# Performance work log

Measured on AMD Instinct MI355X. Metric: run time of the kernel, lower is better.

Reference implementation:

```python
import jax, jax.numpy as jnp
import numpy as np

WINDOW_SIZES = (1, 2, 3)
ALPHA = 0.2          # LeakyReLU negative slope
NEG = -9e15          # mask fill value from the torch code


def _xavier(key, shape, gain=np.sqrt(2.0)):
    fan_in, fan_out = shape[0], shape[1]
    std = gain * np.sqrt(2.0 / (fan_in + fan_out))
    return jax.random.normal(key, shape, jnp.float32) * std


def setup_inputs() -> dict:
    key = jax.random.key(0)
    k1, k2, k3, k4, k5 = jax.random.split(key, 5)
    T, B, D, F = 512, 64, 256, 256  # turns, batch, input_dim, output_dim (must match)
    return {
        "local_semantic_vectors": jax.random.normal(k1, (T, B, D), jnp.float32),
        "input_turns": jax.random.randint(k2, (B,), 0, T),  # turns[bt] <= T-1
        "W": _xavier(k3, (D, F)),
        "a1": _xavier(k4, (F, 1)),
        "a2": _xavier(k5, (F, 1)),
    }


def _window_mean(x, w):
    # x: [B, T, D] -> sliding-window mean over axis 1 (window w), zero-padded at end.
    B, T, D = x.shape
    xp = jnp.pad(x, ((0, 0), (0, w - 1), (0, 0)))
    acc = xp[:, :T]
    for j in range(1, w):  # w <= 3, tiny unrolled loop
        acc = acc + xp[:, j:j + T]
    return acc / w


def reference(local_semantic_vectors, input_turns, W, a1, a2):
    # local_semantic_vectors: [T, B, D] -> [B, T, D]
    x = jnp.swapaxes(local_semantic_vectors, 0, 1)
    B, T, D = x.shape
    t_idx = jnp.arange(T)

    num = jnp.zeros((B, W.shape[1]), jnp.float32)
    vws = jnp.zeros((B,), jnp.float32)  # number of window sizes with cnt > 0

    for w in WINDOW_SIZES:
        # number of valid windows per sample: t runs while w+t-1 <= turns
        cnt = jnp.maximum(input_turns - w + 2, 0)                  # [B]
        valid = t_idx[None, :] < cnt[:, None]                      # [B, T]

        # pooled window vectors, zero beyond cnt (max_turn padded to T;
        # padded rows are fully masked and dropped, so the result matches)
        pooled = jnp.where(valid[:, :, None], _window_mean(x, w), 0.0)  # [B, T, D]

        # GAT-style masked self-attention
        h = pooled @ W                                             # [B, T, F]
        f1 = h @ a1                                                # [B, T, 1]
        f2 = h @ a2                                                # [B, T, 1]
        e = jax.nn.leaky_relu(f1 + jnp.swapaxes(f2, 1, 2), ALPHA)  # [B, T, T]
        mask = valid[:, :, None] & valid[:, None, :]
        attn = jax.nn.softmax(jnp.where(mask, e, NEG), axis=-1)
        h_prime = attn @ h                                         # [B, T, F]

        # mean over the first cnt rows
        denom = jnp.maximum(cnt, 1).astype(jnp.float32)
        inter = (h_prime * valid[:, :, None]).sum(axis=1) / denom[:, None]  # [B, F]

        has = (cnt > 0).astype(jnp.float32)
        num = num + inter * has[:, None]
        vws = vws + has

    # cnt is non-increasing in w, so windows with cnt>0 are exactly the first vws;
    # vws >= 1 always (w=1 gives cnt = turns + 2 >= 2).
    return num / vws[:, None]
```

## Files before the change

kernel.cpp:

```cpp
#include <hip/hip_runtime.h>
#include <math.h>

#define T_DIM 512
#define B_DIM 64
#define D_DIM 256
#define F_DIM 256
#define ALPHA 0.2f
#define L2E 1.44269504089f
#define NEGL -1.0e38f

#define U_OFF 0
#define V_OFF 256
#define P_OFF 512
#define Q_OFF (P_OFF + T_DIM * B_DIM)
#define GG_OFF (Q_OFF + T_DIM * B_DIM)

__global__ __launch_bounds__(256) void g_uv(const float* __restrict__ W,
                                            const float* __restrict__ a1,
                                            const float* __restrict__ a2,
                                            float* __restrict__ ws) {
    int tid = threadIdx.x;
    int wave = tid >> 6, lane = tid & 63;
    int d = blockIdx.x * 4 + wave;
    float4 wv = ((const float4*)(W + (size_t)d * F_DIM))[lane];
    float4 a1v = ((const float4*)a1)[lane];
    float4 a2v = ((const float4*)a2)[lane];
    float p = wv.x * a1v.x + wv.y * a1v.y + wv.z * a1v.z + wv.w * a1v.w;
    float q = wv.x * a2v.x + wv.y * a2v.y + wv.z * a2v.z + wv.w * a2v.w;
    for (int off = 32; off > 0; off >>= 1) {
        p += __shfl_down(p, off);
        q += __shfl_down(q, off);
    }
    if (lane == 0) {
        ws[U_OFF + d] = p;
        ws[V_OFF + d] = q;
    }
}

__global__ __launch_bounds__(512) void g_pq(const float* __restrict__ x,
                                            const int* __restrict__ turns,
                                            float* __restrict__ ws) {
    __shared__ float su[D_DIM], sv[D_DIM];
    int tid = threadIdx.x;
    if (tid < 64) ((float4*)su)[tid] = ((const float4*)(ws + U_OFF))[tid];
    else if (tid < 128) ((float4*)sv)[tid - 64] = ((const float4*)(ws + V_OFF))[tid - 64];
    __syncthreads();
    int lane = tid & 63;
    int gw = blockIdx.x * 8 + (tid >> 6);
    int b = gw & 63;
    int tbase = gw >> 6;
    int tn = turns[b];
    const float4* u4 = (const float4*)su;
    const float4* v4 = (const float4*)sv;
    float4 uv = u4[lane], vv = v4[lane];
#pragma unroll
    for (int k = 0; k < 8; ++k) {
        int t = tbase + k * 64;
        if (t <= tn) {
            size_t r = (size_t)t * B_DIM + b;
            float4 xv = ((const float4*)x)[r * (D_DIM / 4) + lane];
            float pp = xv.x * uv.x + xv.y * uv.y + xv.z * uv.z + xv.w * uv.w;
            float qq = xv.x * vv.x + xv.y * vv.y + xv.z * vv.z + xv.w * vv.w;
            for (int off = 32; off > 0; off >>= 1) {
                pp += __shfl_down(pp, off);
                qq += __shfl_down(qq, off);
            }
            if (lane == 0) {
                ws[P_OFF + b * T_DIM + t] = pp;
                ws[Q_OFF + b * T_DIM + t] = qq;
            }
        }
    }
}

__global__ __launch_bounds__(512) void g_attn(const int* __restrict__ turns,
                                              float* __restrict__ ws,
                                              float* __restrict__ out) {
    int bi = blockIdx.x, tid = threadIdx.x;
    if (bi < 32) out[bi * 512 + tid] = 0.f;
    int b = bi / 3, w = bi % 3 + 1;
    int tn = turns[b];
    int cnt = tn - w + 2;
    if (cnt > T_DIM) cnt = T_DIM;
    float* GG = ws + GG_OFF + ((w - 1) * B_DIM + b) * T_DIM;
    if (cnt <= 0) {
        GG[tid] = 0.f;
        return;
    }
    __shared__ float sp[T_DIM], sq[T_DIM], f2L[T_DIM], red[8];
    __shared__ float2 fc[T_DIM];
    if (tid < 128) {
        ((float4*)sp)[tid] = ((const float4*)(ws + P_OFF + b * T_DIM))[tid];
        ((float4*)sq)[tid] = ((const float4*)(ws + Q_OFF + b * T_DIM))[tid];
    }
    __syncthreads();
    float scale = L2E / (float)w;
    int j = tid;
    float vj;
    if (j < cnt) {
        float a = sq[j];
        if (w > 1) a += sq[j + 1];
        if (w > 2) a += sq[j + 2];
        vj = a * scale;
    } else {
        vj = NEGL;
    }
    f2L[j] = vj;
    float m = vj;
    for (int off = 32; off > 0; off >>= 1) m = fmaxf(m, __shfl_down(m, off));
    if ((tid & 63) == 0) red[tid >> 6] = m;
    __syncthreads();
    float M = red[0];
#pragma unroll
    for (int i2 = 1; i2 < 8; ++i2) M = fmaxf(M, red[i2]);
    if (j < cnt) {
        float a = sp[j];
        if (w > 1) a += sp[j + 1];
        if (w > 2) a += sp[j + 2];
        float f1 = a * scale;
        float s0 = f1 + M;
        float mrow = fmaxf(s0, ALPHA * s0);
        float r = 0.f;
        for (int jj = 0; jj < cnt; ++jj) {
            float s = f1 + f2L[jj];
            s = fmaxf(s, ALPHA * s);
            r += __builtin_amdgcn_exp2f(s - mrow);
        }
        fc[j] = make_float2(f1, mrow + __builtin_amdgcn_logf(r));
    }
    __syncthreads();
    float acc = 0.f;
    if (j < cnt) {
        for (int i = 0; i < cnt; ++i) {
            float2 t2 = fc[i];
            float s = t2.x + vj;
            s = fmaxf(s, ALPHA * s);
            acc += __builtin_amdgcn_exp2f(s - t2.y);
        }
        acc /= (float)cnt;
    }
    GG[j] = (j < cnt) ? acc : 0.f;
}

__global__ __launch_bounds__(512) void g_zout(const float* __restrict__ x,
                                              const int* __restrict__ turns,
                                              const float* __restrict__ W,
                                              const float* __restrict__ ws,
                                              float* __restrict__ out) {
    int b = blockIdx.x >> 2;
    int chunk = blockIdx.x & 3;
    int tn = turns[b];
    int t0 = chunk * 128;
    if (t0 > tn) return;
    int tid = threadIdx.x;
    __shared__ float Cs[128];
    __shared__ float4 zp[512];
    __shared__ float Zs[D_DIM];
    __shared__ float ored[512];
    if (tid < 128) {
        int t = t0 + tid;
        const float* G1 = ws + GG_OFF + (0 * B_DIM + b) * T_DIM;
        const float* G2 = ws + GG_OFF + (1 * B_DIM + b) * T_DIM;
        const float* G3 = ws + GG_OFF + (2 * B_DIM + b) * T_DIM;
        float g2 = G2[t] + (t >= 1 ? G2[t - 1] : 0.f);
        float g3 = G3[t] + (t >= 1 ? G3[t - 1] : 0.f) + (t >= 2 ? G3[t - 2] : 0.f);
        float vws = 1.f + (tn >= 1 ? 1.f : 0.f) + (tn >= 2 ? 1.f : 0.f);
        Cs[tid] = (G1[t] + 0.5f * g2 + (1.0f / 3.0f) * g3) / vws;
    }
    __syncthreads();
    int wave = tid >> 6, lane = tid & 63;
    float4 z = make_float4(0.f, 0.f, 0.f, 0.f);
    {
        int tg = t0 + wave * 16;
        size_t base = ((size_t)tg * B_DIM + b) * (D_DIM / 4) + lane;
#pragma unroll 8
        for (int tt = 0; tt < 16; ++tt) {
            float c = Cs[wave * 16 + tt];
            float4 xv = ((const float4*)x)[base + (size_t)tt * (B_DIM * D_DIM / 4)];
            z.x += c * xv.x; z.y += c * xv.y; z.z += c * xv.z; z.w += c * xv.w;
        }
    }
    zp[tid] = z;
    __syncthreads();
    if (tid < 64) {
        float4 a = zp[tid];
#pragma unroll
        for (int k = 1; k < 8; ++k) {
            float4 bb = zp[k * 64 + tid];
            a.x += bb.x; a.y += bb.y; a.z += bb.z; a.w += bb.w;
        }
        ((float4*)Zs)[tid] = a;
    }
    __syncthreads();
    int f = tid & 255, dh = tid >> 8;
    float acc = 0.f;
#pragma unroll 8
    for (int dd = dh * 128; dd < dh * 128 + 128; ++dd)
        acc += Zs[dd] * W[(size_t)dd * F_DIM + f];
    ored[tid] = acc;
    __syncthreads();
    if (tid < 256)
        atomicAdd(&out[b * F_DIM + tid], ored[tid] + ored[tid + 256]);
}

extern "C" void kernel_launch(void* const* d_in, const int* in_sizes, int n_in,
                              void* d_out, int out_size, void* d_ws, size_t ws_size,
                              hipStream_t stream) {
    const float* x = (const float*)d_in[0];
    const int* turns = (const int*)d_in[1];
    const float* W = (const float*)d_in[2];
    const float* a1 = (const float*)d_in[3];
    const float* a2 = (const float*)d_in[4];
    float* out = (float*)d_out;
    float* ws = (float*)d_ws;

    g_uv<<<B_DIM, 256, 0, stream>>>(W, a1, a2, ws);
    g_pq<<<512, 512, 0, stream>>>(x, turns, ws);
    g_attn<<<B_DIM * 3, 512, 0, stream>>>(turns, ws, out);
    g_zout<<<B_DIM * 4, 512, 0, stream>>>(x, turns, W, ws, out);
}
```

Measured before the change: 55.09 us.

## Split attention kernel into chunked row and column passes with atomic accumulation

Replaces the single per-(batch,window) attention kernel with two kernels that each split the quadratic loop into four 128-wide chunks, giving four times as many blocks. The row pass accumulates softmax denominators into a zeroed workspace with atomics, and the column pass reads them back and atomically accumulates column sums. The goal is better occupancy and shorter serial loops on the 192-block launch. The cost is an extra kernel launch, redundant max reductions in each chunk block, workspace zeroing, and atomic traffic.

```diff
diff --git a/kernel.cpp b/kernel.cpp
--- a/kernel.cpp
+++ b/kernel.cpp
@@ -14,12 +14,17 @@
 #define P_OFF 512
 #define Q_OFF (P_OFF + T_DIM * B_DIM)
 #define GG_OFF (Q_OFF + T_DIM * B_DIM)
+#define R_OFF (GG_OFF + 3 * B_DIM * T_DIM)
 
 __global__ __launch_bounds__(256) void g_uv(const float* __restrict__ W,
                                             const float* __restrict__ a1,
                                             const float* __restrict__ a2,
                                             float* __restrict__ ws) {
     int tid = threadIdx.x;
+    int gid = blockIdx.x * 256 + tid;
+#pragma unroll
+    for (int k = 0; k < 6; ++k)
+        ws[R_OFF + k * 16384 + gid] = 0.f;
     int wave = tid >> 6, lane = tid & 63;
     int d = blockIdx.x * 4 + wave;
     float4 wv = ((const float4*)(W + (size_t)d * F_DIM))[lane];
@@ -42,6 +47,8 @@
                                             float* __restrict__ ws) {
     __shared__ float su[D_DIM], sv[D_DIM];
     int tid = threadIdx.x;
+    int gid = blockIdx.x * 512 + tid;
+    if (gid < 3 * B_DIM * T_DIM) ws[GG_OFF + gid] = 0.f;
     if (tid < 64) ((float4*)su)[tid] = ((const float4*)(ws + U_OFF))[tid];
     else if (tid < 128) ((float4*)sv)[tid - 64] = ((const float4*)(ws + V_OFF))[tid - 64];
     __syncthreads();
@@ -73,22 +80,20 @@
     }
 }
 
-__global__ __launch_bounds__(512) void g_attn(const int* __restrict__ turns,
-                                              float* __restrict__ ws,
-                                              float* __restrict__ out) {
+__global__ __launch_bounds__(512) void g_row(const int* __restrict__ turns,
+                                             float* __restrict__ ws,
+                                             float* __restrict__ out) {
     int bi = blockIdx.x, tid = threadIdx.x;
     if (bi < 32) out[bi * 512 + tid] = 0.f;
-    int b = bi / 3, w = bi % 3 + 1;
+    int b = bi / 12, rem = bi % 12;
+    int w = (rem >> 2) + 1, jc = rem & 3;
     int tn = turns[b];
     int cnt = tn - w + 2;
     if (cnt > T_DIM) cnt = T_DIM;
-    float* GG = ws + GG_OFF + ((w - 1) * B_DIM + b) * T_DIM;
-    if (cnt <= 0) {
-        GG[tid] = 0.f;
-        return;
-    }
+    if (cnt <= 0) return;
+    int j0 = jc * 128;
+    if (j0 >= cnt) return;
     __shared__ float sp[T_DIM], sq[T_DIM], f2L[T_DIM], red[8];
-    __shared__ float2 fc[T_DIM];
     if (tid < 128) {
         ((float4*)sp)[tid] = ((const float4*)(ws + P_OFF + b * T_DIM))[tid];
         ((float4*)sq)[tid] = ((const float4*)(ws + Q_OFF + b * T_DIM))[tid];
@@ -113,33 +118,87 @@
     float M = red[0];
 #pragma unroll
     for (int i2 = 1; i2 < 8; ++i2) M = fmaxf(M, red[i2]);
-    if (j < cnt) {
-        float a = sp[j];
-        if (w > 1) a += sp[j + 1];
-        if (w > 2) a += sp[j + 2];
+    if (tid < cnt) {
+        float a = sp[tid];
+        if (w > 1) a += sp[tid + 1];
+        if (w > 2) a += sp[tid + 2];
         float f1 = a * scale;
         float s0 = f1 + M;
         float mrow = fmaxf(s0, ALPHA * s0);
         float r = 0.f;
-        for (int jj = 0; jj < cnt; ++jj) {
-            float s = f1 + f2L[jj];
+        int j1 = min(j0 + 128, cnt);
+        for (int k = j0; k < j1; ++k) {
+            float s = f1 + f2L[k];
             s = fmaxf(s, ALPHA * s);
             r += __builtin_amdgcn_exp2f(s - mrow);
         }
-        fc[j] = make_float2(f1, mrow + __builtin_amdgcn_logf(r));
-    }
-    __syncthreads();
-    float acc = 0.f;
+        atomicAdd(&ws[R_OFF + ((w - 1) * B_DIM + b) * T_DIM + tid], r);
+    }
+}
+
+__global__ __launch_bounds__(512) void g_col(const int* __restrict__ turns,
+                                             float* __restrict__ ws) {
+    int bi = blockIdx.x, tid = threadIdx.x;
+    int b = bi / 12, rem = bi % 12;
+    int w = (rem >> 2) + 1, ic = rem & 3;
+    int tn = turns[b];
+    int cnt = tn - w + 2;
+    if (cnt > T_DIM) cnt = T_DIM;
+    if (cnt <= 0) return;
+    int i0 = ic * 128;
+    if (i0 >= cnt) return;
+    __shared__ float sp[T_DIM], sq[T_DIM], red[8];
+    __shared__ float2 fc[128];
+    if (tid < 128) {
+        ((float4*)sp)[tid] = ((const float4*)(ws + P_OFF + b * T_DIM))[tid];
+        ((float4*)sq)[tid] = ((const float4*)(ws + Q_OFF + b * T_DIM))[tid];
+    }
+    __syncthreads();
+    float scale = L2E / (float)w;
+    int j = tid;
+    float vj;
     if (j < cnt) {
-        for (int i = 0; i < cnt; ++i) {
-            float2 t2 = fc[i];
+        float a = sq[j];
+        if (w > 1) a += sq[j + 1];
+        if (w > 2) a += sq[j + 2];
+        vj = a * scale;
+    } else {
+        vj = NEGL;
+    }
+    float m = vj;
+    for (int off = 32; off > 0; off >>= 1) m = fmaxf(m, __shfl_down(m, off));
+    if ((tid & 63) == 0) red[tid >> 6] = m;
+    __syncthreads();
+    float M = red[0];
+#pragma unroll
+    for (int i2 = 1; i2 < 8; ++i2) M = fmaxf(M, red[i2]);
+    if (tid < 128) {
+        int i = i0 + tid;
+        float2 v = make_float2(0.f, 0.f);
+        if (i < cnt) {
+            float a = sp[i];
+            if (w > 1) a += sp[i + 1];
+            if (w > 2) a += sp[i + 2];
+            float f1 = a * scale;
+            float s0 = f1 + M;
+            float mrow = fmaxf(s0, ALPHA * s0);
+            float ri = ws[R_OFF + ((w - 1) * B_DIM + b) * T_DIM + i];
+            v = make_float2(f1, mrow + __builtin_amdgcn_logf(ri));
+        }
+        fc[tid] = v;
+    }
+    __syncthreads();
+    if (j < cnt) {
+        float acc = 0.f;
+        int ni = min(128, cnt - i0);
+        for (int k = 0; k < ni; ++k) {
+            float2 t2 = fc[k];
             float s = t2.x + vj;
             s = fmaxf(s, ALPHA * s);
             acc += __builtin_amdgcn_exp2f(s - t2.y);
         }
-        acc /= (float)cnt;
-    }
-    GG[j] = (j < cnt) ? acc : 0.f;
+        atomicAdd(&ws[GG_OFF + ((w - 1) * B_DIM + b) * T_DIM + j], acc / (float)cnt);
+    }
 }
 
 __global__ __launch_bounds__(512) void g_zout(const float* __restrict__ x,
@@ -216,6 +275,7 @@
 
     g_uv<<<B_DIM, 256, 0, stream>>>(W, a1, a2, ws);
     g_pq<<<512, 512, 0, stream>>>(x, turns, ws);
-    g_attn<<<B_DIM * 3, 512, 0, stream>>>(turns, ws, out);
+    g_row<<<B_DIM * 12, 512, 0, stream>>>(turns, ws, out);
+    g_col<<<B_DIM * 12, 512, 0, stream>>>(turns, ws);
     g_zout<<<B_DIM * 4, 512, 0, stream>>>(x, turns, W, ws, out);
 }
```

Result: faster. 53.49 us (-2.9%).
